# Performance work log

Hardware: AMD Instinct MI355X
Metric: run time of the kernel (lower is better)

Reference implementation:

```python
import jax, jax.numpy as jnp
import numpy as np

B, D, H, N, M, S = 64, 256, 512, 16384, 64, 3
EPS = 1e-4


def setup_inputs() -> dict:
    key = jax.random.key(0)
    ks = jax.random.split(key, 20)
    rn = lambda k, shape, sc=1.0: jax.random.normal(k, shape, dtype=jnp.float32) * sc
    z = lambda n: jnp.zeros((n,), jnp.float32)
    sc = 0.05
    return {
        "inp": rn(ks[0], (B, D)),
        "h_tm1": rn(ks[1], (B, H), 0.1),
        "c_tm1": rn(ks[2], (B, H), 0.1),
        "read_tm1": jax.nn.softmax(rn(ks[3], (B, N)), axis=-1),
        "write_tm1": jax.nn.softmax(rn(ks[4], (B, N)), axis=-1),
        "memory": rn(ks[5], (B, N, M), 0.1),
        "W_ih": rn(ks[6], (4 * H, D + M), sc), "b_ih": z(4 * H),
        "W_hh": rn(ks[7], (4 * H, H), sc), "b_hh": z(4 * H),
        "W_rk": rn(ks[8], (M, H), sc), "b_rk": z(M),
        "W_wk": rn(ks[9], (M, H), sc), "b_wk": z(M),
        "W_rc": rn(ks[10], (3, H), sc), "b_rc": z(3),
        "W_wc": rn(ks[11], (3, H), sc), "b_wc": z(3),
        "W_rs": rn(ks[12], (S, H), sc), "b_rs": z(S),
        "W_ws": rn(ks[13], (S, H), sc), "b_ws": z(S),
        "W_w": rn(ks[14], (2 * M, H), sc), "b_w": z(2 * M),
    }


def _head_params(h, Wk, bk, Wc, bc, Ws, bs):
    k = jnp.tanh(h @ Wk.T + bk)                 # [B, M] key
    c = h @ Wc.T + bc                           # [B, 3] beta/g/gamma raw
    s = jax.nn.softmax(h @ Ws.T + bs, axis=-1)  # [B, S] shift dist
    beta = jax.nn.relu(c[:, 0:1]) + EPS
    g = jax.nn.sigmoid(c[:, 1:2])
    gamma = jax.nn.relu(c[:, 2:3]) + 1.0 + EPS
    return k, s, beta, g, gamma


def _address(memory, w_tm1, k, s, beta, g, gamma):
    # content addressing: beta-scaled cosine similarity, softmax over slots
    dot = jnp.einsum('bm,bnm->bn', k, memory)                    # [B, N]
    nM = jnp.sqrt(jnp.sum(memory * memory, axis=-1)) + EPS       # [B, N]
    nk = jnp.sqrt(jnp.sum(k * k, axis=-1, keepdims=True)) + EPS  # [B, 1]
    content = jax.nn.softmax(beta * dot / (nM * nk), axis=-1)
    # interpolation with previous head
    inter = g * content + (1.0 - g) * w_tm1                      # [B, N]
    # circular shift conv: out[j] = sum_r s[r] * inter[(j + r - (S-1)) mod N]
    shifted = jnp.stack([jnp.roll(inter, S - 1 - r, axis=1) for r in range(S)], axis=-1)  # [B, N, S]
    conv = jnp.einsum('bns,bs->bn', shifted, s)
    # sharpening
    sharp = jnp.maximum(conv, 1e-8) ** gamma
    return sharp / jnp.sum(sharp, axis=1, keepdims=True)


def reference(inp, h_tm1, c_tm1, read_tm1, write_tm1, memory,
              W_ih, b_ih, W_hh, b_hh, W_rk, b_rk, W_wk, b_wk,
              W_rc, b_rc, W_wc, b_wc, W_rs, b_rs, W_ws, b_ws, W_w, b_w):
    # read head addressed from previous hidden state
    rk, rs, rbeta, rg, rgamma = _head_params(h_tm1, W_rk, b_rk, W_rc, b_rc, W_rs, b_rs)
    read_head = _address(memory, read_tm1, rk, rs, rbeta, rg, rgamma)
    M_read = jnp.einsum('bn,bnm->bm', read_head, memory)         # [B, M]
    # LSTMCell controller (torch gate order i, f, g, o)
    x = jnp.concatenate([inp, M_read], axis=1)
    gates = x @ W_ih.T + b_ih + h_tm1 @ W_hh.T + b_hh
    i, f, gg, o = jnp.split(gates, 4, axis=1)
    c_t = jax.nn.sigmoid(f) * c_tm1 + jax.nn.sigmoid(i) * jnp.tanh(gg)
    h_t = jax.nn.sigmoid(o) * jnp.tanh(c_t)
    # write head addressed from new hidden state
    wk, ws, wbeta, wg, wgamma = _head_params(h_t, W_wk, b_wk, W_wc, b_wc, W_ws, b_ws)
    write_head = _address(memory, write_tm1, wk, ws, wbeta, wg, wgamma)
    wa = h_t @ W_w.T + b_w
    e = jax.nn.sigmoid(wa[:, :M])                                # erase [B, M]
    a = wa[:, M:]                                                # add   [B, M]
    ww = write_head[:, :, None]                                  # [B, N, 1]
    M_out = memory * (1.0 - ww * e[:, None, :]) + ww * a[:, None, :]
    return (h_t, c_t, read_head, write_head, M_out)
```

## Files before the change

kernel.cpp:

```cpp
#include <hip/hip_runtime.h>
#include <hip/hip_bf16.h>
#include <math.h>

#define B_  64
#define D_  256
#define H_  512
#define N_  16384
#define M_  64
#define S_  3
#define EPS_ 1e-4f

__device__ __forceinline__ float sigmoidf_(float x) { return 1.0f / (1.0f + expf(-x)); }

template <bool WITH_W>
__global__ __launch_bounds__(256) void head_params_kernel(
    const float* __restrict__ h,
    const float* __restrict__ Wk, const float* __restrict__ bk,
    const float* __restrict__ Wc, const float* __restrict__ bc,
    const float* __restrict__ Ws, const float* __restrict__ bs,
    const float* __restrict__ Ww, const float* __restrict__ bw,
    float* __restrict__ k_out, float* __restrict__ nk_out,
    float* __restrict__ s_out,
    float* __restrict__ beta_out, float* __restrict__ g_out, float* __restrict__ gamma_out,
    float* __restrict__ e_out, float* __restrict__ a_out)
{
    const int b = blockIdx.x;
    const int tid = threadIdx.x;
    __shared__ float hs[H_];
    __shared__ float raw[198];
    for (int i = tid; i < H_; i += 256) hs[i] = h[b * H_ + i];
    __syncthreads();
    const int count = WITH_W ? 198 : 70;
    if (tid < count) {
        const float* wrow;
        float bias;
        if (tid < 64)       { wrow = Wk + tid * H_;        bias = bk[tid]; }
        else if (tid < 67)  { wrow = Wc + (tid - 64) * H_; bias = bc[tid - 64]; }
        else if (tid < 70)  { wrow = Ws + (tid - 67) * H_; bias = bs[tid - 67]; }
        else                { wrow = Ww + (tid - 70) * H_; bias = bw[tid - 70]; }
        float acc = 0.f;
        #pragma unroll 8
        for (int i = 0; i < H_; ++i) acc += wrow[i] * hs[i];
        raw[tid] = acc + bias;
    }
    __syncthreads();
    if (tid < 64) {
        float kv = tanhf(raw[tid]);
        k_out[b * 64 + tid] = kv;
        float sq = kv * kv;
        for (int off = 32; off >= 1; off >>= 1) sq += __shfl_xor(sq, off);
        if (tid == 0) nk_out[b] = sqrtf(sq) + EPS_;
    } else if (tid == 64) {
        float c0 = raw[64], c1 = raw[65], c2 = raw[66];
        beta_out[b]  = fmaxf(c0, 0.f) + EPS_;
        g_out[b]     = sigmoidf_(c1);
        gamma_out[b] = fmaxf(c2, 0.f) + 1.f + EPS_;
    } else if (tid == 65) {
        float s0 = raw[67], s1 = raw[68], s2 = raw[69];
        float mx = fmaxf(s0, fmaxf(s1, s2));
        float e0 = expf(s0 - mx), e1 = expf(s1 - mx), e2 = expf(s2 - mx);
        float inv = 1.f / (e0 + e1 + e2);
        s_out[b * 3 + 0] = e0 * inv;
        s_out[b * 3 + 1] = e1 * inv;
        s_out[b * 3 + 2] = e2 * inv;
    }
    if (WITH_W && tid >= 128 && tid < 192) {
        int m = tid - 128;
        e_out[b * 64 + m] = sigmoidf_(raw[70 + m]);
        a_out[b * 64 + m] = raw[134 + m];
    }
}

template <bool COMPUTE_NM>
__global__ __launch_bounds__(256) void dot_kernel(
    const float* __restrict__ memory,
    const float* __restrict__ k,
    float* __restrict__ dot,
    float* __restrict__ nM)
{
    const int tid = threadIdx.x;
    const int lane = tid & 63;
    const int wid = tid >> 6;
    const int grp = lane >> 4;
    const int m16 = lane & 15;
    const int b = blockIdx.x >> 8;
    const int nbase = (blockIdx.x & 255) * 64;
    const float4 k4 = ((const float4*)(k + b * 64))[m16];
    const int slot = wid * 4 + grp;
    const size_t bbase = (size_t)b * N_;
    #pragma unroll
    for (int it = 0; it < 4; ++it) {
        const int n = nbase + it * 16 + slot;
        const float4 m4 = ((const float4*)(memory + (bbase + n) * 64))[m16];
        float d  = m4.x * k4.x + m4.y * k4.y + m4.z * k4.z + m4.w * k4.w;
        float sq = m4.x * m4.x + m4.y * m4.y + m4.z * m4.z + m4.w * m4.w;
        for (int off = 8; off >= 1; off >>= 1) {
            d += __shfl_xor(d, off);
            if (COMPUTE_NM) sq += __shfl_xor(sq, off);
        }
        if (m16 == 0) {
            dot[bbase + n] = d;
            if (COMPUTE_NM) nM[bbase + n] = sqrtf(sq) + EPS_;
        }
    }
}

__global__ __launch_bounds__(1024) void address_kernel(
    const float* __restrict__ dot,
    const float* __restrict__ nM,
    const float* __restrict__ w_tm1,
    const float* __restrict__ nk_a,
    const float* __restrict__ beta_a, const float* __restrict__ g_a,
    const float* __restrict__ gamma_a, const float* __restrict__ s_a,
    float* __restrict__ head_out)
{
    __shared__ float lds[N_];
    const int tid = threadIdx.x;
    const int b = blockIdx.x;
    const size_t base = (size_t)b * N_;
    const float beta = beta_a[b], g = g_a[b], gamma = gamma_a[b], nk = nk_a[b];
    const float s0 = s_a[b * 3 + 0], s1 = s_a[b * 3 + 1], s2 = s_a[b * 3 + 2];

    float lg[16];
    float lmax = -1e30f;
    #pragma unroll
    for (int t = 0; t < 16; ++t) {
        const int n = t * 1024 + tid;
        const float x = beta * dot[base + n] / (nM[base + n] * nk);
        lg[t] = x;
        lmax = fmaxf(lmax, x);
    }
    for (int off = 32; off >= 1; off >>= 1) lmax = fmaxf(lmax, __shfl_xor(lmax, off));
    if ((tid & 63) == 0) lds[tid >> 6] = lmax;
    __syncthreads();
    if (tid == 0) {
        float v = lds[0];
        for (int i = 1; i < 16; ++i) v = fmaxf(v, lds[i]);
        lds[16] = v;
    }
    __syncthreads();
    const float gmax = lds[16];

    float lsum = 0.f;
    #pragma unroll
    for (int t = 0; t < 16; ++t) { lg[t] = expf(lg[t] - gmax); lsum += lg[t]; }
    for (int off = 32; off >= 1; off >>= 1) lsum += __shfl_xor(lsum, off);
    if ((tid & 63) == 0) lds[tid >> 6] = lsum;
    __syncthreads();
    if (tid == 0) {
        float v = 0.f;
        for (int i = 0; i < 16; ++i) v += lds[i];
        lds[16] = v;
    }
    __syncthreads();
    const float inv_sum = 1.f / lds[16];
    __syncthreads();

    #pragma unroll
    for (int t = 0; t < 16; ++t) {
        const int n = t * 1024 + tid;
        lds[n] = g * lg[t] * inv_sum + (1.f - g) * w_tm1[base + n];
    }
    __syncthreads();

    float sh[16];
    float lsum2 = 0.f;
    #pragma unroll
    for (int t = 0; t < 16; ++t) {
        const int n = t * 1024 + tid;
        const float conv = s2 * lds[n] + s1 * lds[(n + N_ - 1) & (N_ - 1)]
                         + s0 * lds[(n + N_ - 2) & (N_ - 1)];
        const float v = powf(fmaxf(conv, 1e-8f), gamma);
        sh[t] = v;
        lsum2 += v;
    }
    __syncthreads();
    for (int off = 32; off >= 1; off >>= 1) lsum2 += __shfl_xor(lsum2, off);
    if ((tid & 63) == 0) lds[tid >> 6] = lsum2;
    __syncthreads();
    if (tid == 0) {
        float v = 0.f;
        for (int i = 0; i < 16; ++i) v += lds[i];
        lds[16] = v;
    }
    __syncthreads();
    const float inv2 = 1.f / lds[16];
    #pragma unroll
    for (int t = 0; t < 16; ++t) head_out[base + t * 1024 + tid] = sh[t] * inv2;
}

__global__ __launch_bounds__(256) void m_read_kernel(
    const float* __restrict__ memory,
    const float* __restrict__ head,
    float* __restrict__ M_read)
{
    const int tid = threadIdx.x;
    const int lane = tid & 63;
    const int wid = tid >> 6;
    const int grp = lane >> 4;
    const int m16 = lane & 15;
    const int b = blockIdx.x >> 6;
    const int nbase = (blockIdx.x & 63) * 256;
    const int slot = wid * 4 + grp;
    const size_t bbase = (size_t)b * N_;
    float4 acc = make_float4(0.f, 0.f, 0.f, 0.f);
    #pragma unroll 4
    for (int it = 0; it < 16; ++it) {
        const int n = nbase + it * 16 + slot;
        const float w = head[bbase + n];
        const float4 m4 = ((const float4*)(memory + (bbase + n) * 64))[m16];
        acc.x += w * m4.x; acc.y += w * m4.y; acc.z += w * m4.z; acc.w += w * m4.w;
    }
    for (int off = 32; off >= 16; off >>= 1) {
        acc.x += __shfl_xor(acc.x, off);
        acc.y += __shfl_xor(acc.y, off);
        acc.z += __shfl_xor(acc.z, off);
        acc.w += __shfl_xor(acc.w, off);
    }
    __shared__ float4 part[64];
    if (lane < 16) part[wid * 16 + lane] = acc;
    __syncthreads();
    if (tid < 16) {
        float4 t = part[tid];
        for (int w = 1; w < 4; ++w) {
            const float4 p = part[w * 16 + tid];
            t.x += p.x; t.y += p.y; t.z += p.z; t.w += p.w;
        }
        atomicAdd(&M_read[b * 64 + tid * 4 + 0], t.x);
        atomicAdd(&M_read[b * 64 + tid * 4 + 1], t.y);
        atomicAdd(&M_read[b * 64 + tid * 4 + 2], t.z);
        atomicAdd(&M_read[b * 64 + tid * 4 + 3], t.w);
    }
}

__global__ __launch_bounds__(256) void gates_kernel(
    const float* __restrict__ inp,
    const float* __restrict__ M_read,
    const float* __restrict__ h_tm1,
    const float* __restrict__ W_ih, const float* __restrict__ b_ih,
    const float* __restrict__ W_hh, const float* __restrict__ b_hh,
    float* __restrict__ gates)
{
    __shared__ __align__(16) float Asm[32][68];
    __shared__ __align__(16) float Bsm[32][68];
    const int tid = threadIdx.x;
    const int tx = tid & 15, ty = tid >> 4;
    const int jbase = blockIdx.x * 64;
    float acc[4][4] = {};
    for (int k0 = 0; k0 < 832; k0 += 32) {
        #pragma unroll
        for (int i = 0; i < 8; ++i) {
            const int e = i * 256 + tid;
            const int kk = e & 31, bb = e >> 5;
            const int kg = k0 + kk;
            float v;
            if (kg < 256)      v = inp[bb * 256 + kg];
            else if (kg < 320) v = M_read[bb * 64 + kg - 256];
            else               v = h_tm1[bb * 512 + kg - 320];
            Asm[kk][bb] = v;
            const int jj = bb;
            const int jg = jbase + jj;
            float w;
            if (kg < 320) w = W_ih[jg * 320 + kg];
            else          w = W_hh[jg * 512 + kg - 320];
            Bsm[kk][jj] = w;
        }
        __syncthreads();
        #pragma unroll
        for (int k = 0; k < 32; ++k) {
            const float4 av = *((const float4*)&Asm[k][ty * 4]);
            const float4 wv = *((const float4*)&Bsm[k][tx * 4]);
            acc[0][0] += av.x * wv.x; acc[0][1] += av.x * wv.y; acc[0][2] += av.x * wv.z; acc[0][3] += av.x * wv.w;
            acc[1][0] += av.y * wv.x; acc[1][1] += av.y * wv.y; acc[1][2] += av.y * wv.z; acc[1][3] += av.y * wv.w;
            acc[2][0] += av.z * wv.x; acc[2][1] += av.z * wv.y; acc[2][2] += av.z * wv.z; acc[2][3] += av.z * wv.w;
            acc[3][0] += av.w * wv.x; acc[3][1] += av.w * wv.y; acc[3][2] += av.w * wv.z; acc[3][3] += av.w * wv.w;
        }
        __syncthreads();
    }
    #pragma unroll
    for (int bi = 0; bi < 4; ++bi) {
        const int b = ty * 4 + bi;
        #pragma unroll
        for (int ji = 0; ji < 4; ++ji) {
            const int j = jbase + tx * 4 + ji;
            gates[b * 2048 + j] = acc[bi][ji] + b_ih[j] + b_hh[j];
        }
    }
}

__global__ __launch_bounds__(256) void lstm_kernel(
    const float* __restrict__ gates,
    const float* __restrict__ c_tm1,
    float* __restrict__ h_out, float* __restrict__ c_out)
{
    const int idx = blockIdx.x * 256 + threadIdx.x;
    const int b = idx >> 9, j = idx & 511;
    const float* gr = gates + b * 2048;
    const float i_ = sigmoidf_(gr[j]);
    const float f_ = sigmoidf_(gr[512 + j]);
    const float g_ = tanhf(gr[1024 + j]);
    const float o_ = sigmoidf_(gr[1536 + j]);
    const float c = f_ * c_tm1[idx] + i_ * g_;
    c_out[idx] = c;
    h_out[idx] = o_ * tanhf(c);
}

__global__ __launch_bounds__(256) void m_out_kernel(
    const float* __restrict__ memory,
    const float* __restrict__ whead,
    const float* __restrict__ e,
    const float* __restrict__ a,
    float* __restrict__ M_out)
{
    const size_t total = (size_t)B_ * N_ * 16;
    const size_t stride = (size_t)gridDim.x * 256;
    for (size_t idx = (size_t)blockIdx.x * 256 + threadIdx.x; idx < total; idx += stride) {
        const size_t nlin = idx >> 4;
        const int m4 = (int)(idx & 15);
        const int b = (int)(nlin >> 14);
        const float w = whead[nlin];
        const float4 ev = ((const float4*)(e + b * 64))[m4];
        const float4 av = ((const float4*)(a + b * 64))[m4];
        const float4 mv = ((const float4*)memory)[idx];
        float4 o;
        o.x = mv.x * (1.f - w * ev.x) + w * av.x;
        o.y = mv.y * (1.f - w * ev.y) + w * av.y;
        o.z = mv.z * (1.f - w * ev.z) + w * av.z;
        o.w = mv.w * (1.f - w * ev.w) + w * av.w;
        ((float4*)M_out)[idx] = o;
    }
}

extern "C" void kernel_launch(void* const* d_in, const int* in_sizes, int n_in,
                              void* d_out, int out_size, void* d_ws, size_t ws_size,
                              hipStream_t stream)
{
    const float* inp       = (const float*)d_in[0];
    const float* h_tm1     = (const float*)d_in[1];
    const float* c_tm1     = (const float*)d_in[2];
    const float* read_tm1  = (const float*)d_in[3];
    const float* write_tm1 = (const float*)d_in[4];
    const float* memory    = (const float*)d_in[5];
    const float* W_ih = (const float*)d_in[6];  const float* b_ih = (const float*)d_in[7];
    const float* W_hh = (const float*)d_in[8];  const float* b_hh = (const float*)d_in[9];
    const float* W_rk = (const float*)d_in[10]; const float* b_rk = (const float*)d_in[11];
    const float* W_wk = (const float*)d_in[12]; const float* b_wk = (const float*)d_in[13];
    const float* W_rc = (const float*)d_in[14]; const float* b_rc = (const float*)d_in[15];
    const float* W_wc = (const float*)d_in[16]; const float* b_wc = (const float*)d_in[17];
    const float* W_rs = (const float*)d_in[18]; const float* b_rs = (const float*)d_in[19];
    const float* W_ws = (const float*)d_in[20]; const float* b_ws = (const float*)d_in[21];
    const float* W_w  = (const float*)d_in[22]; const float* b_w  = (const float*)d_in[23];

    float* out = (float*)d_out;
    float* h_out   = out;
    float* c_out   = out + 32768;
    float* rhead   = out + 65536;
    float* whead   = out + 65536 + 1048576;
    float* Mout    = out + 65536 + 2 * 1048576;

    float* dot_r = rhead;
    float* dot_w = whead;
    float* nM    = Mout;

    float* ws = (float*)d_ws;
    float* gates  = ws;
    float* rk     = ws + 131072;
    float* wk     = ws + 135168;
    float* M_read = ws + 139264;
    float* e_buf  = ws + 143360;
    float* a_buf  = ws + 147456;
    float* rs     = ws + 151552;
    float* wss    = ws + 151744;
    float* rbeta  = ws + 151936;
    float* rg     = ws + 152000;
    float* rgamma = ws + 152064;
    float* rnk    = ws + 152128;
    float* wbeta  = ws + 152192;
    float* wg     = ws + 152256;
    float* wgamma = ws + 152320;
    float* wnk    = ws + 152384;

    hipMemsetAsync(M_read, 0, B_ * M_ * sizeof(float), stream);

    head_params_kernel<false><<<B_, 256, 0, stream>>>(
        h_tm1, W_rk, b_rk, W_rc, b_rc, W_rs, b_rs, nullptr, nullptr,
        rk, rnk, rs, rbeta, rg, rgamma, nullptr, nullptr);
    dot_kernel<true><<<B_ * 256, 256, 0, stream>>>(memory, rk, dot_r, nM);
    address_kernel<<<B_, 1024, 0, stream>>>(dot_r, nM, read_tm1, rnk, rbeta, rg, rgamma, rs, rhead);
    m_read_kernel<<<B_ * 64, 256, 0, stream>>>(memory, rhead, M_read);
    gates_kernel<<<32, 256, 0, stream>>>(inp, M_read, h_tm1, W_ih, b_ih, W_hh, b_hh, gates);
    lstm_kernel<<<128, 256, 0, stream>>>(gates, c_tm1, h_out, c_out);
    head_params_kernel<true><<<B_, 256, 0, stream>>>(
        h_out, W_wk, b_wk, W_wc, b_wc, W_ws, b_ws, W_w, b_w,
        wk, wnk, wss, wbeta, wg, wgamma, e_buf, a_buf);
    dot_kernel<false><<<B_ * 256, 256, 0, stream>>>(memory, wk, dot_w, nullptr);
    address_kernel<<<B_, 1024, 0, stream>>>(dot_w, nM, write_tm1, wnk, wbeta, wg, wgamma, wss, whead);
    m_out_kernel<<<16384, 256, 0, stream>>>(memory, whead, e_buf, a_buf, Mout);
}
```

Measured before the change: 918.7 us.

## Split-K the gates GEMM with atomics and warp-per-row head projections

The gates GEMM is split along K into 13 chunks of 64, which gives 416 blocks instead of 32. Partial sums are accumulated with float atomics into a gates buffer that is zeroed beforehand, and the bias add moves into the LSTM kernel. The head parameter kernel now has each wavefront compute one output row with coalesced weight reads and a shuffle reduction, replacing the single-thread-per-row serial loops. This adds an extra memset, atomic traffic and non-deterministic summation order. Both kernels were small, latency-bound parts of a memory-dominated pipeline.

```diff
diff --git a/kernel.cpp b/kernel.cpp
--- a/kernel.cpp
+++ b/kernel.cpp
@@ -26,24 +26,30 @@
 {
     const int b = blockIdx.x;
     const int tid = threadIdx.x;
-    __shared__ float hs[H_];
+    const int lane = tid & 63;
+    const int wid = tid >> 6;
     __shared__ float raw[198];
-    for (int i = tid; i < H_; i += 256) hs[i] = h[b * H_ + i];
-    __syncthreads();
+
+    float h8[8];
+    #pragma unroll
+    for (int j = 0; j < 8; ++j) h8[j] = h[b * H_ + lane + 64 * j];
+
     const int count = WITH_W ? 198 : 70;
-    if (tid < count) {
+    for (int r = wid; r < count; r += 4) {
         const float* wrow;
         float bias;
-        if (tid < 64)       { wrow = Wk + tid * H_;        bias = bk[tid]; }
-        else if (tid < 67)  { wrow = Wc + (tid - 64) * H_; bias = bc[tid - 64]; }
-        else if (tid < 70)  { wrow = Ws + (tid - 67) * H_; bias = bs[tid - 67]; }
-        else                { wrow = Ww + (tid - 70) * H_; bias = bw[tid - 70]; }
+        if (r < 64)       { wrow = Wk + r * H_;        bias = bk[r]; }
+        else if (r < 67)  { wrow = Wc + (r - 64) * H_; bias = bc[r - 64]; }
+        else if (r < 70)  { wrow = Ws + (r - 67) * H_; bias = bs[r - 67]; }
+        else              { wrow = Ww + (r - 70) * H_; bias = bw[r - 70]; }
         float acc = 0.f;
-        #pragma unroll 8
-        for (int i = 0; i < H_; ++i) acc += wrow[i] * hs[i];
-        raw[tid] = acc + bias;
-    }
-    __syncthreads();
+        #pragma unroll
+        for (int j = 0; j < 8; ++j) acc += wrow[lane + 64 * j] * h8[j];
+        for (int off = 32; off >= 1; off >>= 1) acc += __shfl_xor(acc, off);
+        if (lane == 0) raw[r] = acc + bias;
+    }
+    __syncthreads();
+
     if (tid < 64) {
         float kv = tanhf(raw[tid]);
         k_out[b * 64 + tid] = kv;
@@ -233,73 +239,84 @@
     }
 }
 
-__global__ __launch_bounds__(256) void gates_kernel(
+__global__ __launch_bounds__(256) void gates_splitk_kernel(
     const float* __restrict__ inp,
     const float* __restrict__ M_read,
     const float* __restrict__ h_tm1,
-    const float* __restrict__ W_ih, const float* __restrict__ b_ih,
-    const float* __restrict__ W_hh, const float* __restrict__ b_hh,
+    const float* __restrict__ W_ih,
+    const float* __restrict__ W_hh,
     float* __restrict__ gates)
 {
-    __shared__ __align__(16) float Asm[32][68];
-    __shared__ __align__(16) float Bsm[32][68];
+    __shared__ __align__(16) float Xsm[64][68];
+    __shared__ __align__(16) float Wsm[64][68];
     const int tid = threadIdx.x;
+    const int jb = blockIdx.x & 31;
+    const int c  = blockIdx.x >> 5;
+    const int j0 = jb * 64;
+
+    #pragma unroll
+    for (int i = 0; i < 4; ++i) {
+        const int e = i * 256 + tid;
+        const int row = e >> 4;
+        const int c4 = e & 15;
+        const float* xrow;
+        if (c < 4)       xrow = inp    + row * 256 + c * 64;
+        else if (c == 4) xrow = M_read + row * 64;
+        else             xrow = h_tm1  + row * 512 + (c - 5) * 64;
+        const float4 v = ((const float4*)xrow)[c4];
+        const int kl = c4 * 4;
+        Xsm[kl + 0][row] = v.x; Xsm[kl + 1][row] = v.y;
+        Xsm[kl + 2][row] = v.z; Xsm[kl + 3][row] = v.w;
+    }
+    #pragma unroll
+    for (int i = 0; i < 4; ++i) {
+        const int e = i * 256 + tid;
+        const int row = e >> 4;
+        const int c4 = e & 15;
+        const float* wrow;
+        if (c < 5) wrow = W_ih + (j0 + row) * 320 + c * 64;
+        else       wrow = W_hh + (j0 + row) * 512 + (c - 5) * 64;
+        const float4 v = ((const float4*)wrow)[c4];
+        const int kl = c4 * 4;
+        Wsm[kl + 0][row] = v.x; Wsm[kl + 1][row] = v.y;
+        Wsm[kl + 2][row] = v.z; Wsm[kl + 3][row] = v.w;
+    }
+    __syncthreads();
+
     const int tx = tid & 15, ty = tid >> 4;
-    const int jbase = blockIdx.x * 64;
     float acc[4][4] = {};
-    for (int k0 = 0; k0 < 832; k0 += 32) {
-        #pragma unroll
-        for (int i = 0; i < 8; ++i) {
-            const int e = i * 256 + tid;
-            const int kk = e & 31, bb = e >> 5;
-            const int kg = k0 + kk;
-            float v;
-            if (kg < 256)      v = inp[bb * 256 + kg];
-            else if (kg < 320) v = M_read[bb * 64 + kg - 256];
-            else               v = h_tm1[bb * 512 + kg - 320];
-            Asm[kk][bb] = v;
-            const int jj = bb;
-            const int jg = jbase + jj;
-            float w;
-            if (kg < 320) w = W_ih[jg * 320 + kg];
-            else          w = W_hh[jg * 512 + kg - 320];
-            Bsm[kk][jj] = w;
-        }
-        __syncthreads();
-        #pragma unroll
-        for (int k = 0; k < 32; ++k) {
-            const float4 av = *((const float4*)&Asm[k][ty * 4]);
-            const float4 wv = *((const float4*)&Bsm[k][tx * 4]);
-            acc[0][0] += av.x * wv.x; acc[0][1] += av.x * wv.y; acc[0][2] += av.x * wv.z; acc[0][3] += av.x * wv.w;
-            acc[1][0] += av.y * wv.x; acc[1][1] += av.y * wv.y; acc[1][2] += av.y * wv.z; acc[1][3] += av.y * wv.w;
-            acc[2][0] += av.z * wv.x; acc[2][1] += av.z * wv.y; acc[2][2] += av.z * wv.z; acc[2][3] += av.z * wv.w;
-            acc[3][0] += av.w * wv.x; acc[3][1] += av.w * wv.y; acc[3][2] += av.w * wv.z; acc[3][3] += av.w * wv.w;
-        }
-        __syncthreads();
+    #pragma unroll
+    for (int k = 0; k < 64; ++k) {
+        const float4 av = *((const float4*)&Xsm[k][ty * 4]);
+        const float4 wv = *((const float4*)&Wsm[k][tx * 4]);
+        acc[0][0] += av.x * wv.x; acc[0][1] += av.x * wv.y; acc[0][2] += av.x * wv.z; acc[0][3] += av.x * wv.w;
+        acc[1][0] += av.y * wv.x; acc[1][1] += av.y * wv.y; acc[1][2] += av.y * wv.z; acc[1][3] += av.y * wv.w;
+        acc[2][0] += av.z * wv.x; acc[2][1] += av.z * wv.y; acc[2][2] += av.z * wv.z; acc[2][3] += av.z * wv.w;
+        acc[3][0] += av.w * wv.x; acc[3][1] += av.w * wv.y; acc[3][2] += av.w * wv.z; acc[3][3] += av.w * wv.w;
     }
     #pragma unroll
     for (int bi = 0; bi < 4; ++bi) {
         const int b = ty * 4 + bi;
         #pragma unroll
         for (int ji = 0; ji < 4; ++ji) {
-            const int j = jbase + tx * 4 + ji;
-            gates[b * 2048 + j] = acc[bi][ji] + b_ih[j] + b_hh[j];
+            atomicAdd(&gates[b * 2048 + j0 + tx * 4 + ji], acc[bi][ji]);
         }
     }
 }
 
 __global__ __launch_bounds__(256) void lstm_kernel(
     const float* __restrict__ gates,
+    const float* __restrict__ b_ih, const float* __restrict__ b_hh,
     const float* __restrict__ c_tm1,
     float* __restrict__ h_out, float* __restrict__ c_out)
 {
     const int idx = blockIdx.x * 256 + threadIdx.x;
     const int b = idx >> 9, j = idx & 511;
     const float* gr = gates + b * 2048;
-    const float i_ = sigmoidf_(gr[j]);
-    const float f_ = sigmoidf_(gr[512 + j]);
-    const float g_ = tanhf(gr[1024 + j]);
-    const float o_ = sigmoidf_(gr[1536 + j]);
+    const float i_ = sigmoidf_(gr[j]        + b_ih[j]        + b_hh[j]);
+    const float f_ = sigmoidf_(gr[512 + j]  + b_ih[512 + j]  + b_hh[512 + j]);
+    const float g_ = tanhf(   gr[1024 + j] + b_ih[1024 + j] + b_hh[1024 + j]);
+    const float o_ = sigmoidf_(gr[1536 + j] + b_ih[1536 + j] + b_hh[1536 + j]);
     const float c = f_ * c_tm1[idx] + i_ * g_;
     c_out[idx] = c;
     h_out[idx] = o_ * tanhf(c);
@@ -381,6 +398,7 @@
     float* wnk    = ws + 152384;
 
     hipMemsetAsync(M_read, 0, B_ * M_ * sizeof(float), stream);
+    hipMemsetAsync(gates, 0, B_ * 4 * H_ * sizeof(float), stream);
 
     head_params_kernel<false><<<B_, 256, 0, stream>>>(
         h_tm1, W_rk, b_rk, W_rc, b_rc, W_rs, b_rs, nullptr, nullptr,
@@ -388,8 +406,8 @@
     dot_kernel<true><<<B_ * 256, 256, 0, stream>>>(memory, rk, dot_r, nM);
     address_kernel<<<B_, 1024, 0, stream>>>(dot_r, nM, read_tm1, rnk, rbeta, rg, rgamma, rs, rhead);
     m_read_kernel<<<B_ * 64, 256, 0, stream>>>(memory, rhead, M_read);
-    gates_kernel<<<32, 256, 0, stream>>>(inp, M_read, h_tm1, W_ih, b_ih, W_hh, b_hh, gates);
-    lstm_kernel<<<128, 256, 0, stream>>>(gates, c_tm1, h_out, c_out);
+    gates_splitk_kernel<<<13 * 32, 256, 0, stream>>>(inp, M_read, h_tm1, W_ih, W_hh, gates);
+    lstm_kernel<<<128, 256, 0, stream>>>(gates, b_ih, b_hh, c_tm1, h_out, c_out);
     head_params_kernel<true><<<B_, 256, 0, stream>>>(
         h_out, W_wk, b_wk, W_wc, b_wc, W_ws, b_ws, W_w, b_w,
         wk, wnk, wss, wbeta, wg, wgamma, e_buf, a_buf);
```

After: 785.8 us. 1.17x faster.
